# Kernel tuning notes

Hardware: AMD Instinct MI355X
Metric: run time of the kernel (lower is better)

The kernel has to match this reference:

```python
import jax, jax.numpy as jnp
import numpy as np

SEQ_LEN = 8192
EMBED_DIM = 768
OUTPUT_DIM = 64


def setup_inputs() -> dict:
    key = jax.random.key(0)
    k_in, k_q, k_k, k_v = jax.random.split(key, 4)
    inputs = jax.random.normal(k_in, (SEQ_LEN, EMBED_DIM), dtype=jnp.float32)
    W_Q = jax.random.normal(k_q, (EMBED_DIM, OUTPUT_DIM), dtype=jnp.float32)
    W_K = jax.random.normal(k_k, (EMBED_DIM, OUTPUT_DIM), dtype=jnp.float32)
    W_V = jax.random.normal(k_v, (EMBED_DIM, OUTPUT_DIM), dtype=jnp.float32)
    return {"inputs": inputs, "W_Q": W_Q, "W_K": W_K, "W_V": W_V}


def reference(inputs, W_Q, W_K, W_V):
    # inputs: [N, E]; weights: [E, D]
    queries = inputs @ W_Q              # [N, D]
    keys = inputs @ W_K                 # [N, D]
    values = inputs @ W_V               # [N, D]
    scale = values.shape[-1] ** 0.5     # sqrt(output_dim), as in the original
    scores = queries @ keys.T           # [N, N] -- full score matrix, as original
    weights = jax.nn.softmax(scores / scale, axis=-1)
    context = weights @ values          # [N, D]
    return context
```

## Files before the change

kernel.cpp:

```cpp
#include <hip/hip_runtime.h>
#include <hip/hip_fp16.h>

#define N_SEQ 8192
#define E_DIM 768
#define D_OUT 64
#define PADK 68
#define SCALE_LOG2 0.18033688011112042f

typedef __attribute__((ext_vector_type(8)))  short s16x8;
typedef __attribute__((ext_vector_type(4)))  float f32x4;
typedef __attribute__((ext_vector_type(16))) float f32x16;

static __device__ __forceinline__ unsigned short f2bf(float f) {
    union { float f; unsigned int u; } v; v.f = f;
    unsigned int r = v.u + 0x7FFFu + ((v.u >> 16) & 1u);
    return (unsigned short)(r >> 16);
}
static __device__ __forceinline__ float bf2f(unsigned short h) {
    union { float f; unsigned int u; } v; v.u = ((unsigned int)h) << 16; return v.f;
}
static __device__ __forceinline__ unsigned int packbf(float a, float b) {
    union { float f; unsigned int u; } x, y; x.f = a; y.f = b;
    return (y.u & 0xFFFF0000u) | (x.u >> 16);
}
static __device__ __forceinline__ s16x8 gfrag(const unsigned short* p) {
    union { uint4 u; s16x8 s; } r; r.u = *(const uint4*)p; return r.s;
}
static __device__ __forceinline__ s16x8 ldsfrag(const unsigned short* p) {
    union { uint2 u[2]; s16x8 s; } r;
    r.u[0] = *(const uint2*)(p);
    r.u[1] = *(const uint2*)(p + 4);
    return r.s;
}
static __device__ __forceinline__ void st32(unsigned short* d, uint4 a, uint4 b) {
    uint2* p = (uint2*)d;
    p[0] = make_uint2(a.x, a.y); p[1] = make_uint2(a.z, a.w);
    p[2] = make_uint2(b.x, b.y); p[3] = make_uint2(b.z, b.w);
}

__global__ __launch_bounds__(256) void prep_w(const float* __restrict__ WQ,
                                              const float* __restrict__ WK,
                                              const float* __restrict__ WV,
                                              unsigned short* __restrict__ Wthi,
                                              unsigned short* __restrict__ Wtlo) {
    int idx = blockIdx.x * 256 + threadIdx.x;
    if (idx >= 192 * E_DIM) return;
    int n = idx / E_DIM;
    int k = idx - n * E_DIM;
    float v;
    if (n < 64)       v = WQ[k * 64 + n];
    else if (n < 128) v = WK[k * 64 + (n - 64)];
    else              v = WV[k * 64 + (n - 128)];
    unsigned short hb = f2bf(v);
    Wthi[idx] = hb;
    Wtlo[idx] = f2bf(v - bf2f(hb));
}

__global__ __launch_bounds__(256) void prep_x(const float* __restrict__ X,
                                              unsigned short* __restrict__ Xhi,
                                              unsigned short* __restrict__ Xlo) {
    int idx = blockIdx.x * 256 + threadIdx.x;
    float4 v = ((const float4*)X)[idx];
    ushort4 hi, lo;
    hi.x = f2bf(v.x); lo.x = f2bf(v.x - bf2f(hi.x));
    hi.y = f2bf(v.y); lo.y = f2bf(v.y - bf2f(hi.y));
    hi.z = f2bf(v.z); lo.z = f2bf(v.z - bf2f(hi.z));
    hi.w = f2bf(v.w); lo.w = f2bf(v.w - bf2f(hi.w));
    ((ushort4*)Xhi)[idx] = hi;
    ((ushort4*)Xlo)[idx] = lo;
}

__global__ __launch_bounds__(256, 4) void proj_qkv(const unsigned short* __restrict__ Xhi,
                                                   const unsigned short* __restrict__ Xlo,
                                                   const unsigned short* __restrict__ Wthi,
                                                   const unsigned short* __restrict__ Wtlo,
                                                   unsigned short* __restrict__ Qhi,
                                                   unsigned short* __restrict__ Qlo,
                                                   unsigned short* __restrict__ Khi,
                                                   unsigned short* __restrict__ Klo,
                                                   unsigned short* __restrict__ Vt) {
    int tid  = threadIdx.x;
    int wv   = tid >> 6;
    int lane = tid & 63;
    int id   = blockIdx.x * 4 + wv;
    int mt   = id >> 2;
    int c    = id & 3;
    int m0 = mt * 16, n0 = c * 16;
    int lr = lane & 15, lk = lane >> 4;

    f32x4 aQ, aK, aV;
    #pragma unroll
    for (int i = 0; i < 4; ++i) { aQ[i] = 0.f; aK[i] = 0.f; aV[i] = 0.f; }

    const unsigned short* xh  = Xhi  + (size_t)(m0 + lr) * E_DIM + lk * 8;
    const unsigned short* xl  = Xlo  + (size_t)(m0 + lr) * E_DIM + lk * 8;
    const unsigned short* wqh = Wthi + (size_t)(n0 + lr) * E_DIM + lk * 8;
    const unsigned short* wql = Wtlo + (size_t)(n0 + lr) * E_DIM + lk * 8;
    const unsigned short* wkh = Wthi + (size_t)(64 + n0 + lr) * E_DIM + lk * 8;
    const unsigned short* wkl = Wtlo + (size_t)(64 + n0 + lr) * E_DIM + lk * 8;
    const unsigned short* wvh = Wthi + (size_t)(128 + n0 + lr) * E_DIM + lk * 8;

    #pragma unroll 2
    for (int ks = 0; ks < E_DIM / 32; ++ks) {
        int kb = ks * 32;
        s16x8 ah = gfrag(xh + kb);
        s16x8 al = gfrag(xl + kb);
        s16x8 bqh = gfrag(wqh + kb);
        s16x8 bql = gfrag(wql + kb);
        s16x8 bkh = gfrag(wkh + kb);
        s16x8 bkl = gfrag(wkl + kb);
        s16x8 bvh = gfrag(wvh + kb);
        aQ = __builtin_amdgcn_mfma_f32_16x16x32_bf16(ah, bqh, aQ, 0, 0, 0);
        aK = __builtin_amdgcn_mfma_f32_16x16x32_bf16(ah, bkh, aK, 0, 0, 0);
        aV = __builtin_amdgcn_mfma_f32_16x16x32_bf16(ah, bvh, aV, 0, 0, 0);
        aQ = __builtin_amdgcn_mfma_f32_16x16x32_bf16(ah, bql, aQ, 0, 0, 0);
        aK = __builtin_amdgcn_mfma_f32_16x16x32_bf16(ah, bkl, aK, 0, 0, 0);
        aQ = __builtin_amdgcn_mfma_f32_16x16x32_bf16(al, bqh, aQ, 0, 0, 0);
        aK = __builtin_amdgcn_mfma_f32_16x16x32_bf16(al, bkh, aK, 0, 0, 0);
    }

    #pragma unroll
    for (int r = 0; r < 4; ++r) {
        int grow = m0 + lk * 4 + r, gcol = n0 + lr;
        float q = aQ[r] * SCALE_LOG2;
        unsigned short hb = f2bf(q);
        Qhi[(size_t)grow * 64 + gcol] = hb;
        Qlo[(size_t)grow * 64 + gcol] = f2bf(q - bf2f(hb));
        float v = aK[r];
        hb = f2bf(v);
        Khi[(size_t)grow * 64 + gcol] = hb;
        Klo[(size_t)grow * 64 + gcol] = f2bf(v - bf2f(hb));
    }
    ushort4 pk;
    pk.x = f2bf(aV[0]); pk.y = f2bf(aV[1]);
    pk.z = f2bf(aV[2]); pk.w = f2bf(aV[3]);
    *(ushort4*)(Vt + (size_t)(n0 + lr) * N_SEQ + m0 + lk * 4) = pk;
}

__global__ __launch_bounds__(256, 3) void attn(const unsigned short* __restrict__ Qhi,
                                               const unsigned short* __restrict__ Qlo,
                                               const unsigned short* __restrict__ Khi,
                                               const unsigned short* __restrict__ Klo,
                                               const unsigned short* __restrict__ Vt,
                                               float* __restrict__ Opart,
                                               float* __restrict__ mpart,
                                               float* __restrict__ lpart,
                                               int chunk) {
    __shared__ unsigned short sK[128 * PADK];
    __shared__ unsigned short sV [64 * PADK];

    int tid = threadIdx.x, wv = tid >> 6, lane = tid & 63;
    int lrow = lane & 31, lh = lane >> 5;
    int c = blockIdx.x, qb = blockIdx.y;
    int q0 = qb * 128 + wv * 32;

    s16x8 qh[4], ql[4];
    #pragma unroll
    for (int ks = 0; ks < 4; ++ks) {
        int kb = ks * 16 + lh * 8;
        qh[ks] = gfrag(Qhi + (size_t)(q0 + lrow) * 64 + kb);
        ql[ks] = gfrag(Qlo + (size_t)(q0 + lrow) * 64 + kb);
    }

    f32x16 O0, O1;
    #pragma unroll
    for (int i = 0; i < 16; ++i) { O0[i] = 0.f; O1[i] = 0.f; }
    float mrow = -1e30f, lrun = 0.f;

    int steps = chunk >> 6;
    int srow = tid >> 2, sseg = tid & 3;

    uint4 rA0, rA1, rB0, rB1, rC0, rC1;
    {
        int j1 = c * chunk;
        const uint4* ps = (const uint4*)(Khi + ((size_t)(j1 + srow) * 64 + sseg * 16));
        rA0 = ps[0]; rA1 = ps[1];
        ps = (const uint4*)(Klo + ((size_t)(j1 + srow) * 64 + sseg * 16));
        rB0 = ps[0]; rB1 = ps[1];
        ps = (const uint4*)(Vt + ((size_t)srow * N_SEQ + j1 + sseg * 16));
        rC0 = ps[0]; rC1 = ps[1];
    }

    for (int it = 0; it < steps; ++it) {
        __syncthreads();
        st32(sK + srow * PADK + sseg * 16, rA0, rA1);
        st32(sK + (64 + srow) * PADK + sseg * 16, rB0, rB1);
        st32(sV + srow * PADK + sseg * 16, rC0, rC1);
        __syncthreads();

        if (it + 1 < steps) {
            int j1 = c * chunk + (it + 1) * 64;
            const uint4* ps = (const uint4*)(Khi + ((size_t)(j1 + srow) * 64 + sseg * 16));
            rA0 = ps[0]; rA1 = ps[1];
            ps = (const uint4*)(Klo + ((size_t)(j1 + srow) * 64 + sseg * 16));
            rB0 = ps[0]; rB1 = ps[1];
            ps = (const uint4*)(Vt + ((size_t)srow * N_SEQ + j1 + sseg * 16));
            rC0 = ps[0]; rC1 = ps[1];
        }

        f32x16 s0, s1;
        #pragma unroll
        for (int i = 0; i < 16; ++i) { s0[i] = 0.f; s1[i] = 0.f; }
        #pragma unroll
        for (int ks = 0; ks < 4; ++ks) {
            int kb = ks * 16 + lh * 8;
            s16x8 b0h = ldsfrag(sK + (size_t)lrow * PADK + kb);
            s16x8 b0l = ldsfrag(sK + (size_t)(64 + lrow) * PADK + kb);
            s0 = __builtin_amdgcn_mfma_f32_32x32x16_bf16(b0h, qh[ks], s0, 0, 0, 0);
            s0 = __builtin_amdgcn_mfma_f32_32x32x16_bf16(b0l, qh[ks], s0, 0, 0, 0);
            s0 = __builtin_amdgcn_mfma_f32_32x32x16_bf16(b0h, ql[ks], s0, 0, 0, 0);
            s16x8 b1h = ldsfrag(sK + (size_t)(32 + lrow) * PADK + kb);
            s16x8 b1l = ldsfrag(sK + (size_t)(96 + lrow) * PADK + kb);
            s1 = __builtin_amdgcn_mfma_f32_32x32x16_bf16(b1h, qh[ks], s1, 0, 0, 0);
            s1 = __builtin_amdgcn_mfma_f32_32x32x16_bf16(b1l, qh[ks], s1, 0, 0, 0);
            s1 = __builtin_amdgcn_mfma_f32_32x32x16_bf16(b1h, ql[ks], s1, 0, 0, 0);
        }

        float rm = s0[0];
        #pragma unroll
        for (int i = 1; i < 16; ++i) rm = fmaxf(rm, s0[i]);
        #pragma unroll
        for (int i = 0; i < 16; ++i) rm = fmaxf(rm, s1[i]);
        rm = fmaxf(rm, __shfl_xor(rm, 32, 64));
        float mn  = fmaxf(mrow, rm);
        float alf = exp2f(mrow - mn);
        mrow = mn;

        float psum = 0.f;
        #pragma unroll
        for (int i = 0; i < 16; ++i) { s0[i] = exp2f(s0[i] - mn); psum += s0[i]; }
        #pragma unroll
        for (int i = 0; i < 16; ++i) { s1[i] = exp2f(s1[i] - mn); psum += s1[i]; }
        lrun = lrun * alf + psum;

        unsigned int I[16], J[16];
        #pragma unroll
        for (int q4 = 0; q4 < 4; ++q4) {
            I[2 * q4]     = packbf(s0[4 * q4],     s0[4 * q4 + 1]);
            I[2 * q4 + 1] = packbf(s0[4 * q4 + 2], s0[4 * q4 + 3]);
            I[8 + 2 * q4]     = packbf(s1[4 * q4],     s1[4 * q4 + 1]);
            I[8 + 2 * q4 + 1] = packbf(s1[4 * q4 + 2], s1[4 * q4 + 3]);
        }
        #pragma unroll
        for (int i = 0; i < 16; ++i) J[i] = (unsigned int)__shfl_xor((int)I[i], 32, 64);
        s16x8 a[4];
        #pragma unroll
        for (int ks = 0; ks < 4; ++ks) {
            int b = (ks >> 1) * 8 + (ks & 1) * 4;
            union { unsigned int u[4]; s16x8 s; } fa;
            fa.u[0] = lh ? J[b + 2] : I[b];
            fa.u[1] = lh ? J[b + 3] : I[b + 1];
            fa.u[2] = lh ? I[b + 2] : J[b];
            fa.u[3] = lh ? I[b + 3] : J[b + 1];
            a[ks] = fa.s;
        }

        #pragma unroll
        for (int r = 0; r < 16; ++r) {
            int qr = (r & 3) + 8 * (r >> 2) + 4 * lh;
            float af = __shfl(alf, qr, 64);
            O0[r] *= af; O1[r] *= af;
        }

        #pragma unroll
        for (int ks = 0; ks < 4; ++ks) {
            int kb = ks * 16 + lh * 8;
            s16x8 b0 = ldsfrag(sV + (size_t)lrow * PADK + kb);
            s16x8 b1 = ldsfrag(sV + (size_t)(32 + lrow) * PADK + kb);
            O0 = __builtin_amdgcn_mfma_f32_32x32x16_bf16(a[ks], b0, O0, 0, 0, 0);
            O1 = __builtin_amdgcn_mfma_f32_32x32x16_bf16(a[ks], b1, O1, 0, 0, 0);
        }
    }

    #pragma unroll
    for (int r = 0; r < 16; ++r) {
        int row = (r & 3) + 8 * (r >> 2) + 4 * lh;
        int grow = q0 + row;
        size_t ob = ((size_t)c * N_SEQ + grow) * 64;
        Opart[ob + lrow]      = O0[r];
        Opart[ob + 32 + lrow] = O1[r];
    }
    float lfull = lrun + __shfl_xor(lrun, 32, 64);
    if (lane < 32) {
        int grow = q0 + lrow;
        mpart[c * N_SEQ + grow] = mrow;
        lpart[c * N_SEQ + grow] = lfull;
    }
}

__global__ __launch_bounds__(256) void combine(const float* __restrict__ Opart,
                                               const float* __restrict__ mpart,
                                               const float* __restrict__ lpart,
                                               float* __restrict__ out,
                                               int nsplit) {
    int idx = blockIdx.x * 256 + threadIdx.x;
    int row = idx >> 4, d4 = idx & 15;
    float M = -1e30f;
    for (int c = 0; c < nsplit; ++c) M = fmaxf(M, mpart[c * N_SEQ + row]);
    float4 num = make_float4(0.f, 0.f, 0.f, 0.f);
    float den = 0.f;
    for (int c = 0; c < nsplit; ++c) {
        float w = exp2f(mpart[c * N_SEQ + row] - M);
        den += w * lpart[c * N_SEQ + row];
        float4 o = ((const float4*)Opart)[((size_t)c * N_SEQ + row) * 16 + d4];
        num.x += w * o.x; num.y += w * o.y; num.z += w * o.z; num.w += w * o.w;
    }
    float inv = 1.0f / den;
    num.x *= inv; num.y *= inv; num.z *= inv; num.w *= inv;
    ((float4*)out)[idx] = num;
}

extern "C" void kernel_launch(void* const* d_in, const int* in_sizes, int n_in,
                              void* d_out, int out_size, void* d_ws, size_t ws_size,
                              hipStream_t stream) {
    const float* X  = (const float*)d_in[0];
    const float* WQ = (const float*)d_in[1];
    const float* WK = (const float*)d_in[2];
    const float* WV = (const float*)d_in[3];
    float* out = (float*)d_out;

    const size_t szQK = (size_t)N_SEQ * 64 * 2;
    const size_t szW  = (size_t)192 * E_DIM * 2;
    const size_t szX  = (size_t)N_SEQ * E_DIM * 2;
    char* p = (char*)d_ws;
    unsigned short* Qhi = (unsigned short*)p; p += szQK;
    unsigned short* Qlo = (unsigned short*)p; p += szQK;
    unsigned short* Khi = (unsigned short*)p; p += szQK;
    unsigned short* Klo = (unsigned short*)p; p += szQK;
    unsigned short* Vt  = (unsigned short*)p; p += szQK;
    unsigned short* Wthi = (unsigned short*)p; p += szW;
    unsigned short* Wtlo = (unsigned short*)p; p += szW;
    unsigned short* Xhi = (unsigned short*)p; p += szX;
    unsigned short* Xlo = (unsigned short*)p; p += szX;
    size_t base = (size_t)(p - (char*)d_ws);
    size_t per  = (size_t)N_SEQ * 64 * 4 + 2 * (size_t)N_SEQ * 4;
    int nsplit = 16;
    while (nsplit > 1 && base + (size_t)nsplit * per > ws_size) nsplit >>= 1;
    float* mpart = (float*)p; p += (size_t)nsplit * N_SEQ * 4;
    float* lpart = (float*)p; p += (size_t)nsplit * N_SEQ * 4;
    float* Opart = (float*)p;

    int chunk = N_SEQ / nsplit;

    prep_w<<<(192 * E_DIM + 255) / 256, 256, 0, stream>>>(WQ, WK, WV, Wthi, Wtlo);
    prep_x<<<(N_SEQ * E_DIM / 4) / 256, 256, 0, stream>>>(X, Xhi, Xlo);
    proj_qkv<<<512, 256, 0, stream>>>(Xhi, Xlo, Wthi, Wtlo, Qhi, Qlo, Khi, Klo, Vt);
    attn<<<dim3(nsplit, N_SEQ / 128), 256, 0, stream>>>(Qhi, Qlo, Khi, Klo, Vt,
                                                        Opart, mpart, lpart, chunk);
    combine<<<(N_SEQ * 16 + 255) / 256, 256, 0, stream>>>(Opart, mpart, lpart, out, nsplit);
}
```

Before: 178.3 us.

## Drop LDS staging in attention, store partials in bf16, merge prep kernels

```diff
diff --git a/kernel.cpp b/kernel.cpp
--- a/kernel.cpp
+++ b/kernel.cpp
@@ -4,7 +4,6 @@
 #define N_SEQ 8192
 #define E_DIM 768
 #define D_OUT 64
-#define PADK 68
 #define SCALE_LOG2 0.18033688011112042f
 
 typedef __attribute__((ext_vector_type(8)))  short s16x8;
@@ -26,48 +25,39 @@
 static __device__ __forceinline__ s16x8 gfrag(const unsigned short* p) {
     union { uint4 u; s16x8 s; } r; r.u = *(const uint4*)p; return r.s;
 }
-static __device__ __forceinline__ s16x8 ldsfrag(const unsigned short* p) {
-    union { uint2 u[2]; s16x8 s; } r;
-    r.u[0] = *(const uint2*)(p);
-    r.u[1] = *(const uint2*)(p + 4);
-    return r.s;
-}
-static __device__ __forceinline__ void st32(unsigned short* d, uint4 a, uint4 b) {
-    uint2* p = (uint2*)d;
-    p[0] = make_uint2(a.x, a.y); p[1] = make_uint2(a.z, a.w);
-    p[2] = make_uint2(b.x, b.y); p[3] = make_uint2(b.z, b.w);
-}
-
-__global__ __launch_bounds__(256) void prep_w(const float* __restrict__ WQ,
-                                              const float* __restrict__ WK,
-                                              const float* __restrict__ WV,
-                                              unsigned short* __restrict__ Wthi,
-                                              unsigned short* __restrict__ Wtlo) {
-    int idx = blockIdx.x * 256 + threadIdx.x;
-    if (idx >= 192 * E_DIM) return;
-    int n = idx / E_DIM;
-    int k = idx - n * E_DIM;
-    float v;
-    if (n < 64)       v = WQ[k * 64 + n];
-    else if (n < 128) v = WK[k * 64 + (n - 64)];
-    else              v = WV[k * 64 + (n - 128)];
-    unsigned short hb = f2bf(v);
-    Wthi[idx] = hb;
-    Wtlo[idx] = f2bf(v - bf2f(hb));
-}
-
-__global__ __launch_bounds__(256) void prep_x(const float* __restrict__ X,
-                                              unsigned short* __restrict__ Xhi,
-                                              unsigned short* __restrict__ Xlo) {
-    int idx = blockIdx.x * 256 + threadIdx.x;
-    float4 v = ((const float4*)X)[idx];
-    ushort4 hi, lo;
-    hi.x = f2bf(v.x); lo.x = f2bf(v.x - bf2f(hi.x));
-    hi.y = f2bf(v.y); lo.y = f2bf(v.y - bf2f(hi.y));
-    hi.z = f2bf(v.z); lo.z = f2bf(v.z - bf2f(hi.z));
-    hi.w = f2bf(v.w); lo.w = f2bf(v.w - bf2f(hi.w));
-    ((ushort4*)Xhi)[idx] = hi;
-    ((ushort4*)Xlo)[idx] = lo;
+
+#define NXB 6144
+__global__ __launch_bounds__(256) void prep(const float* __restrict__ X,
+                                            const float* __restrict__ WQ,
+                                            const float* __restrict__ WK,
+                                            const float* __restrict__ WV,
+                                            unsigned short* __restrict__ Xhi,
+                                            unsigned short* __restrict__ Xlo,
+                                            unsigned short* __restrict__ Wthi,
+                                            unsigned short* __restrict__ Wtlo) {
+    int b = blockIdx.x;
+    if (b < NXB) {
+        int idx = b * 256 + threadIdx.x;
+        float4 v = ((const float4*)X)[idx];
+        ushort4 hi, lo;
+        hi.x = f2bf(v.x); lo.x = f2bf(v.x - bf2f(hi.x));
+        hi.y = f2bf(v.y); lo.y = f2bf(v.y - bf2f(hi.y));
+        hi.z = f2bf(v.z); lo.z = f2bf(v.z - bf2f(hi.z));
+        hi.w = f2bf(v.w); lo.w = f2bf(v.w - bf2f(hi.w));
+        ((ushort4*)Xhi)[idx] = hi;
+        ((ushort4*)Xlo)[idx] = lo;
+    } else {
+        int idx = (b - NXB) * 256 + threadIdx.x;
+        int n = idx / E_DIM;
+        int k = idx - n * E_DIM;
+        float v;
+        if (n < 64)       v = WQ[k * 64 + n];
+        else if (n < 128) v = WK[k * 64 + (n - 64)];
+        else              v = WV[k * 64 + (n - 128)];
+        unsigned short hb = f2bf(v);
+        Wthi[idx] = hb;
+        Wtlo[idx] = f2bf(v - bf2f(hb));
+    }
 }
 
 __global__ __launch_bounds__(256, 4) void proj_qkv(const unsigned short* __restrict__ Xhi,
@@ -142,13 +132,10 @@
                                                const unsigned short* __restrict__ Khi,
                                                const unsigned short* __restrict__ Klo,
                                                const unsigned short* __restrict__ Vt,
-                                               float* __restrict__ Opart,
+                                               unsigned short* __restrict__ Opart,
                                                float* __restrict__ mpart,
                                                float* __restrict__ lpart,
                                                int chunk) {
-    __shared__ unsigned short sK[128 * PADK];
-    __shared__ unsigned short sV [64 * PADK];
-
     int tid = threadIdx.x, wv = tid >> 6, lane = tid & 63;
     int lrow = lane & 31, lh = lane >> 5;
     int c = blockIdx.x, qb = blockIdx.y;
@@ -168,52 +155,29 @@
     float mrow = -1e30f, lrun = 0.f;
 
     int steps = chunk >> 6;
-    int srow = tid >> 2, sseg = tid & 3;
-
-    uint4 rA0, rA1, rB0, rB1, rC0, rC1;
-    {
-        int j1 = c * chunk;
-        const uint4* ps = (const uint4*)(Khi + ((size_t)(j1 + srow) * 64 + sseg * 16));
-        rA0 = ps[0]; rA1 = ps[1];
-        ps = (const uint4*)(Klo + ((size_t)(j1 + srow) * 64 + sseg * 16));
-        rB0 = ps[0]; rB1 = ps[1];
-        ps = (const uint4*)(Vt + ((size_t)srow * N_SEQ + j1 + sseg * 16));
-        rC0 = ps[0]; rC1 = ps[1];
-    }
 
     for (int it = 0; it < steps; ++it) {
-        __syncthreads();
-        st32(sK + srow * PADK + sseg * 16, rA0, rA1);
-        st32(sK + (64 + srow) * PADK + sseg * 16, rB0, rB1);
-        st32(sV + srow * PADK + sseg * 16, rC0, rC1);
-        __syncthreads();
-
-        if (it + 1 < steps) {
-            int j1 = c * chunk + (it + 1) * 64;
-            const uint4* ps = (const uint4*)(Khi + ((size_t)(j1 + srow) * 64 + sseg * 16));
-            rA0 = ps[0]; rA1 = ps[1];
-            ps = (const uint4*)(Klo + ((size_t)(j1 + srow) * 64 + sseg * 16));
-            rB0 = ps[0]; rB1 = ps[1];
-            ps = (const uint4*)(Vt + ((size_t)srow * N_SEQ + j1 + sseg * 16));
-            rC0 = ps[0]; rC1 = ps[1];
-        }
+        int j0 = c * chunk + it * 64;
 
         f32x16 s0, s1;
         #pragma unroll
         for (int i = 0; i < 16; ++i) { s0[i] = 0.f; s1[i] = 0.f; }
+        const unsigned short* kh0 = Khi + (size_t)(j0 + lrow) * 64 + lh * 8;
+        const unsigned short* kl0 = Klo + (size_t)(j0 + lrow) * 64 + lh * 8;
+        const unsigned short* kh1 = kh0 + 32 * 64;
+        const unsigned short* kl1 = kl0 + 32 * 64;
         #pragma unroll
         for (int ks = 0; ks < 4; ++ks) {
-            int kb = ks * 16 + lh * 8;
-            s16x8 b0h = ldsfrag(sK + (size_t)lrow * PADK + kb);
-            s16x8 b0l = ldsfrag(sK + (size_t)(64 + lrow) * PADK + kb);
-            s0 = __builtin_amdgcn_mfma_f32_32x32x16_bf16(b0h, qh[ks], s0, 0, 0, 0);
-            s0 = __builtin_amdgcn_mfma_f32_32x32x16_bf16(b0l, qh[ks], s0, 0, 0, 0);
-            s0 = __builtin_amdgcn_mfma_f32_32x32x16_bf16(b0h, ql[ks], s0, 0, 0, 0);
-            s16x8 b1h = ldsfrag(sK + (size_t)(32 + lrow) * PADK + kb);
-            s16x8 b1l = ldsfrag(sK + (size_t)(96 + lrow) * PADK + kb);
-            s1 = __builtin_amdgcn_mfma_f32_32x32x16_bf16(b1h, qh[ks], s1, 0, 0, 0);
-            s1 = __builtin_amdgcn_mfma_f32_32x32x16_bf16(b1l, qh[ks], s1, 0, 0, 0);
-            s1 = __builtin_amdgcn_mfma_f32_32x32x16_bf16(b1h, ql[ks], s1, 0, 0, 0);
+            s16x8 a0h = gfrag(kh0 + ks * 16);
+            s16x8 a0l = gfrag(kl0 + ks * 16);
+            s16x8 a1h = gfrag(kh1 + ks * 16);
+            s16x8 a1l = gfrag(kl1 + ks * 16);
+            s0 = __builtin_amdgcn_mfma_f32_32x32x16_bf16(a0h, qh[ks], s0, 0, 0, 0);
+            s0 = __builtin_amdgcn_mfma_f32_32x32x16_bf16(a0l, qh[ks], s0, 0, 0, 0);
+            s0 = __builtin_amdgcn_mfma_f32_32x32x16_bf16(a0h, ql[ks], s0, 0, 0, 0);
+            s1 = __builtin_amdgcn_mfma_f32_32x32x16_bf16(a1h, qh[ks], s1, 0, 0, 0);
+            s1 = __builtin_amdgcn_mfma_f32_32x32x16_bf16(a1l, qh[ks], s1, 0, 0, 0);
+            s1 = __builtin_amdgcn_mfma_f32_32x32x16_bf16(a1h, ql[ks], s1, 0, 0, 0);
         }
 
         float rm = s0[0];
@@ -236,8 +200,8 @@
         unsigned int I[16], J[16];
         #pragma unroll
         for (int q4 = 0; q4 < 4; ++q4) {
-            I[2 * q4]     = packbf(s0[4 * q4],     s0[4 * q4 + 1]);
-            I[2 * q4 + 1] = packbf(s0[4 * q4 + 2], s0[4 * q4 + 3]);
+            I[2 * q4]         = packbf(s0[4 * q4],     s0[4 * q4 + 1]);
+            I[2 * q4 + 1]     = packbf(s0[4 * q4 + 2], s0[4 * q4 + 3]);
             I[8 + 2 * q4]     = packbf(s1[4 * q4],     s1[4 * q4 + 1]);
             I[8 + 2 * q4 + 1] = packbf(s1[4 * q4 + 2], s1[4 * q4 + 3]);
         }
@@ -255,18 +219,21 @@
             a[ks] = fa.s;
         }
 
-        #pragma unroll
-        for (int r = 0; r < 16; ++r) {
-            int qr = (r & 3) + 8 * (r >> 2) + 4 * lh;
-            float af = __shfl(alf, qr, 64);
-            O0[r] *= af; O1[r] *= af;
-        }
-
+        if (__any(alf != 1.0f)) {
+            #pragma unroll
+            for (int r = 0; r < 16; ++r) {
+                int qr = (r & 3) + 8 * (r >> 2) + 4 * lh;
+                float af = __shfl(alf, qr, 64);
+                O0[r] *= af; O1[r] *= af;
+            }
+        }
+
+        const unsigned short* vb0 = Vt + (size_t)lrow * N_SEQ + j0 + lh * 8;
+        const unsigned short* vb1 = vb0 + 32 * N_SEQ;
         #pragma unroll
         for (int ks = 0; ks < 4; ++ks) {
-            int kb = ks * 16 + lh * 8;
-            s16x8 b0 = ldsfrag(sV + (size_t)lrow * PADK + kb);
-            s16x8 b1 = ldsfrag(sV + (size_t)(32 + lrow) * PADK + kb);
+            s16x8 b0 = gfrag(vb0 + ks * 16);
+            s16x8 b1 = gfrag(vb1 + ks * 16);
             O0 = __builtin_amdgcn_mfma_f32_32x32x16_bf16(a[ks], b0, O0, 0, 0, 0);
             O1 = __builtin_amdgcn_mfma_f32_32x32x16_bf16(a[ks], b1, O1, 0, 0, 0);
         }
@@ -277,8 +244,8 @@
         int row = (r & 3) + 8 * (r >> 2) + 4 * lh;
         int grow = q0 + row;
         size_t ob = ((size_t)c * N_SEQ + grow) * 64;
-        Opart[ob + lrow]      = O0[r];
-        Opart[ob + 32 + lrow] = O1[r];
+        Opart[ob + lrow]      = f2bf(O0[r]);
+        Opart[ob + 32 + lrow] = f2bf(O1[r]);
     }
     float lfull = lrun + __shfl_xor(lrun, 32, 64);
     if (lane < 32) {
@@ -288,7 +255,7 @@
     }
 }
 
-__global__ __launch_bounds__(256) void combine(const float* __restrict__ Opart,
+__global__ __launch_bounds__(256) void combine(const unsigned short* __restrict__ Opart,
                                                const float* __restrict__ mpart,
                                                const float* __restrict__ lpart,
                                                float* __restrict__ out,
@@ -296,14 +263,17 @@
     int idx = blockIdx.x * 256 + threadIdx.x;
     int row = idx >> 4, d4 = idx & 15;
     float M = -1e30f;
+    #pragma unroll 4
     for (int c = 0; c < nsplit; ++c) M = fmaxf(M, mpart[c * N_SEQ + row]);
     float4 num = make_float4(0.f, 0.f, 0.f, 0.f);
     float den = 0.f;
+    #pragma unroll 4
     for (int c = 0; c < nsplit; ++c) {
         float w = exp2f(mpart[c * N_SEQ + row] - M);
         den += w * lpart[c * N_SEQ + row];
-        float4 o = ((const float4*)Opart)[((size_t)c * N_SEQ + row) * 16 + d4];
-        num.x += w * o.x; num.y += w * o.y; num.z += w * o.z; num.w += w * o.w;
+        ushort4 o = *(const ushort4*)(Opart + ((size_t)c * N_SEQ + row) * 64 + d4 * 4);
+        num.x += w * bf2f(o.x); num.y += w * bf2f(o.y);
+        num.z += w * bf2f(o.z); num.w += w * bf2f(o.w);
     }
     float inv = 1.0f / den;
     num.x *= inv; num.y *= inv; num.z *= inv; num.w *= inv;
@@ -333,17 +303,17 @@
     unsigned short* Xhi = (unsigned short*)p; p += szX;
     unsigned short* Xlo = (unsigned short*)p; p += szX;
     size_t base = (size_t)(p - (char*)d_ws);
-    size_t per  = (size_t)N_SEQ * 64 * 4 + 2 * (size_t)N_SEQ * 4;
+    size_t per  = (size_t)N_SEQ * 64 * 2 + 2 * (size_t)N_SEQ * 4;
     int nsplit = 16;
     while (nsplit > 1 && base + (size_t)nsplit * per > ws_size) nsplit >>= 1;
     float* mpart = (float*)p; p += (size_t)nsplit * N_SEQ * 4;
     float* lpart = (float*)p; p += (size_t)nsplit * N_SEQ * 4;
-    float* Opart = (float*)p;
+    unsigned short* Opart = (unsigned short*)p;
 
     int chunk = N_SEQ / nsplit;
 
-    prep_w<<<(192 * E_DIM + 255) / 256, 256, 0, stream>>>(WQ, WK, WV, Wthi, Wtlo);
-    prep_x<<<(N_SEQ * E_DIM / 4) / 256, 256, 0, stream>>>(X, Xhi, Xlo);
+    prep<<<NXB + (192 * E_DIM) / 256, 256, 0, stream>>>(X, WQ, WK, WV,
+                                                        Xhi, Xlo, Wthi, Wtlo);
     proj_qkv<<<512, 256, 0, stream>>>(Xhi, Xlo, Wthi, Wtlo, Qhi, Qlo, Khi, Klo, Vt);
     attn<<<dim3(nsplit, N_SEQ / 128), 256, 0, stream>>>(Qhi, Qlo, Khi, Klo, Vt,
                                                         Opart, mpart, lpart, chunk);
```

After: 228.5 us. +28.2%, slower.

## Fuse X bf16 split into projection, bf16 partials, skip unit rescale, more splits

Applied to the files above, without the earlier changes.

```diff
diff --git a/kernel.cpp b/kernel.cpp
--- a/kernel.cpp
+++ b/kernel.cpp
@@ -44,7 +44,6 @@
                                               unsigned short* __restrict__ Wthi,
                                               unsigned short* __restrict__ Wtlo) {
     int idx = blockIdx.x * 256 + threadIdx.x;
-    if (idx >= 192 * E_DIM) return;
     int n = idx / E_DIM;
     int k = idx - n * E_DIM;
     float v;
@@ -56,22 +55,7 @@
     Wtlo[idx] = f2bf(v - bf2f(hb));
 }
 
-__global__ __launch_bounds__(256) void prep_x(const float* __restrict__ X,
-                                              unsigned short* __restrict__ Xhi,
-                                              unsigned short* __restrict__ Xlo) {
-    int idx = blockIdx.x * 256 + threadIdx.x;
-    float4 v = ((const float4*)X)[idx];
-    ushort4 hi, lo;
-    hi.x = f2bf(v.x); lo.x = f2bf(v.x - bf2f(hi.x));
-    hi.y = f2bf(v.y); lo.y = f2bf(v.y - bf2f(hi.y));
-    hi.z = f2bf(v.z); lo.z = f2bf(v.z - bf2f(hi.z));
-    hi.w = f2bf(v.w); lo.w = f2bf(v.w - bf2f(hi.w));
-    ((ushort4*)Xhi)[idx] = hi;
-    ((ushort4*)Xlo)[idx] = lo;
-}
-
-__global__ __launch_bounds__(256, 4) void proj_qkv(const unsigned short* __restrict__ Xhi,
-                                                   const unsigned short* __restrict__ Xlo,
+__global__ __launch_bounds__(256, 2) void proj_qkv(const float* __restrict__ X,
                                                    const unsigned short* __restrict__ Wthi,
                                                    const unsigned short* __restrict__ Wtlo,
                                                    unsigned short* __restrict__ Qhi,
@@ -82,9 +66,8 @@
     int tid  = threadIdx.x;
     int wv   = tid >> 6;
     int lane = tid & 63;
-    int id   = blockIdx.x * 4 + wv;
-    int mt   = id >> 2;
-    int c    = id & 3;
+    int mt   = blockIdx.x;
+    int c    = wv;
     int m0 = mt * 16, n0 = c * 16;
     int lr = lane & 15, lk = lane >> 4;
 
@@ -92,8 +75,7 @@
     #pragma unroll
     for (int i = 0; i < 4; ++i) { aQ[i] = 0.f; aK[i] = 0.f; aV[i] = 0.f; }
 
-    const unsigned short* xh  = Xhi  + (size_t)(m0 + lr) * E_DIM + lk * 8;
-    const unsigned short* xl  = Xlo  + (size_t)(m0 + lr) * E_DIM + lk * 8;
+    const float* xb = X + (size_t)(m0 + lr) * E_DIM + lk * 8;
     const unsigned short* wqh = Wthi + (size_t)(n0 + lr) * E_DIM + lk * 8;
     const unsigned short* wql = Wtlo + (size_t)(n0 + lr) * E_DIM + lk * 8;
     const unsigned short* wkh = Wthi + (size_t)(64 + n0 + lr) * E_DIM + lk * 8;
@@ -103,20 +85,30 @@
     #pragma unroll 2
     for (int ks = 0; ks < E_DIM / 32; ++ks) {
         int kb = ks * 32;
-        s16x8 ah = gfrag(xh + kb);
-        s16x8 al = gfrag(xl + kb);
+        union { float4 f[2]; float s[8]; unsigned int u[8]; } xv;
+        xv.f[0] = *(const float4*)(xb + kb);
+        xv.f[1] = *(const float4*)(xb + kb + 4);
+        union { unsigned int u[4]; s16x8 s; } ah, al;
+        #pragma unroll
+        for (int j = 0; j < 4; ++j) {
+            union { unsigned int u; float f; } h0, h1;
+            h0.u = xv.u[2 * j]     & 0xFFFF0000u;
+            h1.u = xv.u[2 * j + 1] & 0xFFFF0000u;
+            ah.u[j] = (xv.u[2 * j] >> 16) | (xv.u[2 * j + 1] & 0xFFFF0000u);
+            al.u[j] = packbf(xv.s[2 * j] - h0.f, xv.s[2 * j + 1] - h1.f);
+        }
         s16x8 bqh = gfrag(wqh + kb);
         s16x8 bql = gfrag(wql + kb);
         s16x8 bkh = gfrag(wkh + kb);
         s16x8 bkl = gfrag(wkl + kb);
         s16x8 bvh = gfrag(wvh + kb);
-        aQ = __builtin_amdgcn_mfma_f32_16x16x32_bf16(ah, bqh, aQ, 0, 0, 0);
-        aK = __builtin_amdgcn_mfma_f32_16x16x32_bf16(ah, bkh, aK, 0, 0, 0);
-        aV = __builtin_amdgcn_mfma_f32_16x16x32_bf16(ah, bvh, aV, 0, 0, 0);
-        aQ = __builtin_amdgcn_mfma_f32_16x16x32_bf16(ah, bql, aQ, 0, 0, 0);
-        aK = __builtin_amdgcn_mfma_f32_16x16x32_bf16(ah, bkl, aK, 0, 0, 0);
-        aQ = __builtin_amdgcn_mfma_f32_16x16x32_bf16(al, bqh, aQ, 0, 0, 0);
-        aK = __builtin_amdgcn_mfma_f32_16x16x32_bf16(al, bkh, aK, 0, 0, 0);
+        aQ = __builtin_amdgcn_mfma_f32_16x16x32_bf16(ah.s, bqh, aQ, 0, 0, 0);
+        aK = __builtin_amdgcn_mfma_f32_16x16x32_bf16(ah.s, bkh, aK, 0, 0, 0);
+        aV = __builtin_amdgcn_mfma_f32_16x16x32_bf16(ah.s, bvh, aV, 0, 0, 0);
+        aQ = __builtin_amdgcn_mfma_f32_16x16x32_bf16(ah.s, bql, aQ, 0, 0, 0);
+        aK = __builtin_amdgcn_mfma_f32_16x16x32_bf16(ah.s, bkl, aK, 0, 0, 0);
+        aQ = __builtin_amdgcn_mfma_f32_16x16x32_bf16(al.s, bqh, aQ, 0, 0, 0);
+        aK = __builtin_amdgcn_mfma_f32_16x16x32_bf16(al.s, bkh, aK, 0, 0, 0);
     }
 
     #pragma unroll
@@ -142,7 +134,7 @@
                                                const unsigned short* __restrict__ Khi,
                                                const unsigned short* __restrict__ Klo,
                                                const unsigned short* __restrict__ Vt,
-                                               float* __restrict__ Opart,
+                                               unsigned short* __restrict__ Opart,
                                                float* __restrict__ mpart,
                                                float* __restrict__ lpart,
                                                int chunk) {
@@ -236,8 +228,8 @@
         unsigned int I[16], J[16];
         #pragma unroll
         for (int q4 = 0; q4 < 4; ++q4) {
-            I[2 * q4]     = packbf(s0[4 * q4],     s0[4 * q4 + 1]);
-            I[2 * q4 + 1] = packbf(s0[4 * q4 + 2], s0[4 * q4 + 3]);
+            I[2 * q4]         = packbf(s0[4 * q4],     s0[4 * q4 + 1]);
+            I[2 * q4 + 1]     = packbf(s0[4 * q4 + 2], s0[4 * q4 + 3]);
             I[8 + 2 * q4]     = packbf(s1[4 * q4],     s1[4 * q4 + 1]);
             I[8 + 2 * q4 + 1] = packbf(s1[4 * q4 + 2], s1[4 * q4 + 3]);
         }
@@ -255,11 +247,13 @@
             a[ks] = fa.s;
         }
 
-        #pragma unroll
-        for (int r = 0; r < 16; ++r) {
-            int qr = (r & 3) + 8 * (r >> 2) + 4 * lh;
-            float af = __shfl(alf, qr, 64);
-            O0[r] *= af; O1[r] *= af;
+        if (__any(alf != 1.0f)) {
+            #pragma unroll
+            for (int r = 0; r < 16; ++r) {
+                int qr = (r & 3) + 8 * (r >> 2) + 4 * lh;
+                float af = __shfl(alf, qr, 64);
+                O0[r] *= af; O1[r] *= af;
+            }
         }
 
         #pragma unroll
@@ -277,8 +271,8 @@
         int row = (r & 3) + 8 * (r >> 2) + 4 * lh;
         int grow = q0 + row;
         size_t ob = ((size_t)c * N_SEQ + grow) * 64;
-        Opart[ob + lrow]      = O0[r];
-        Opart[ob + 32 + lrow] = O1[r];
+        Opart[ob + lrow]      = f2bf(O0[r]);
+        Opart[ob + 32 + lrow] = f2bf(O1[r]);
     }
     float lfull = lrun + __shfl_xor(lrun, 32, 64);
     if (lane < 32) {
@@ -288,7 +282,7 @@
     }
 }
 
-__global__ __launch_bounds__(256) void combine(const float* __restrict__ Opart,
+__global__ __launch_bounds__(256) void combine(const unsigned short* __restrict__ Opart,
                                                const float* __restrict__ mpart,
                                                const float* __restrict__ lpart,
                                                float* __restrict__ out,
@@ -296,14 +290,17 @@
     int idx = blockIdx.x * 256 + threadIdx.x;
     int row = idx >> 4, d4 = idx & 15;
     float M = -1e30f;
+    #pragma unroll 4
     for (int c = 0; c < nsplit; ++c) M = fmaxf(M, mpart[c * N_SEQ + row]);
     float4 num = make_float4(0.f, 0.f, 0.f, 0.f);
     float den = 0.f;
+    #pragma unroll 4
     for (int c = 0; c < nsplit; ++c) {
         float w = exp2f(mpart[c * N_SEQ + row] - M);
         den += w * lpart[c * N_SEQ + row];
-        float4 o = ((const float4*)Opart)[((size_t)c * N_SEQ + row) * 16 + d4];
-        num.x += w * o.x; num.y += w * o.y; num.z += w * o.z; num.w += w * o.w;
+        ushort4 o = *(const ushort4*)(Opart + ((size_t)c * N_SEQ + row) * 64 + d4 * 4);
+        num.x += w * bf2f(o.x); num.y += w * bf2f(o.y);
+        num.z += w * bf2f(o.z); num.w += w * bf2f(o.w);
     }
     float inv = 1.0f / den;
     num.x *= inv; num.y *= inv; num.z *= inv; num.w *= inv;
@@ -321,7 +318,6 @@
 
     const size_t szQK = (size_t)N_SEQ * 64 * 2;
     const size_t szW  = (size_t)192 * E_DIM * 2;
-    const size_t szX  = (size_t)N_SEQ * E_DIM * 2;
     char* p = (char*)d_ws;
     unsigned short* Qhi = (unsigned short*)p; p += szQK;
     unsigned short* Qlo = (unsigned short*)p; p += szQK;
@@ -330,21 +326,18 @@
     unsigned short* Vt  = (unsigned short*)p; p += szQK;
     unsigned short* Wthi = (unsigned short*)p; p += szW;
     unsigned short* Wtlo = (unsigned short*)p; p += szW;
-    unsigned short* Xhi = (unsigned short*)p; p += szX;
-    unsigned short* Xlo = (unsigned short*)p; p += szX;
     size_t base = (size_t)(p - (char*)d_ws);
-    size_t per  = (size_t)N_SEQ * 64 * 4 + 2 * (size_t)N_SEQ * 4;
-    int nsplit = 16;
+    size_t per  = (size_t)N_SEQ * 64 * 2 + 2 * (size_t)N_SEQ * 4;
+    int nsplit = 32;
     while (nsplit > 1 && base + (size_t)nsplit * per > ws_size) nsplit >>= 1;
     float* mpart = (float*)p; p += (size_t)nsplit * N_SEQ * 4;
     float* lpart = (float*)p; p += (size_t)nsplit * N_SEQ * 4;
-    float* Opart = (float*)p;
+    unsigned short* Opart = (unsigned short*)p;
 
     int chunk = N_SEQ / nsplit;
 
-    prep_w<<<(192 * E_DIM + 255) / 256, 256, 0, stream>>>(WQ, WK, WV, Wthi, Wtlo);
-    prep_x<<<(N_SEQ * E_DIM / 4) / 256, 256, 0, stream>>>(X, Xhi, Xlo);
-    proj_qkv<<<512, 256, 0, stream>>>(Xhi, Xlo, Wthi, Wtlo, Qhi, Qlo, Khi, Klo, Vt);
+    prep_w<<<(192 * E_DIM) / 256, 256, 0, stream>>>(WQ, WK, WV, Wthi, Wtlo);
+    proj_qkv<<<512, 256, 0, stream>>>(X, Wthi, Wtlo, Qhi, Qlo, Khi, Klo, Vt);
     attn<<<dim3(nsplit, N_SEQ / 128), 256, 0, stream>>>(Qhi, Qlo, Khi, Klo, Vt,
                                                         Opart, mpart, lpart, chunk);
     combine<<<(N_SEQ * 16 + 255) / 256, 256, 0, stream>>>(Opart, mpart, lpart, out, nsplit);
```

Measured after the change: 195.3 us. +9.5%, slower.
